# Kernel tuning notes

Measured on AMD Instinct MI355X. Metric: run time of the kernel, lower is better.

## Reference

```python
import jax, jax.numpy as jnp
import numpy as np

IN_CH = 512
HID_CH = 512
NUM_HEADS = HID_CH // 32  # 16 heads, 32 channels each
GN_GROUPS = 32
EPS = 1e-6


def group_norm(x, scale, bias):
    # x: (b, c, t); GroupNorm over (channels-in-group, t)
    b, c, t = x.shape
    xg = x.reshape(b, GN_GROUPS, c // GN_GROUPS, t)
    mean = xg.mean(axis=(2, 3), keepdims=True)
    var = xg.var(axis=(2, 3), keepdims=True)
    xg = (xg - mean) * jax.lax.rsqrt(var + EPS)
    return xg.reshape(b, c, t) * scale[None, :, None] + bias[None, :, None]


def setup_inputs() -> dict:
    key = jax.random.key(0)
    ks = jax.random.split(key, 12)
    b, t = 16, 8192
    s = 0.02
    return {
        "x": jax.random.normal(ks[0], (b, IN_CH, t), dtype=jnp.float32),
        "gn_scale": jnp.ones((IN_CH,), jnp.float32),
        "gn_bias": jnp.zeros((IN_CH,), jnp.float32),
        "wq": jax.random.normal(ks[1], (HID_CH, IN_CH), jnp.float32) * s,
        "bq": jnp.zeros((HID_CH,), jnp.float32),
        "wk": jax.random.normal(ks[2], (HID_CH, IN_CH), jnp.float32) * s,
        "bk": jnp.zeros((HID_CH,), jnp.float32),
        "wv": jax.random.normal(ks[3], (HID_CH, IN_CH), jnp.float32) * s,
        "bv": jnp.zeros((HID_CH,), jnp.float32),
        "wp": jax.random.normal(ks[4], (IN_CH, HID_CH), jnp.float32) * s,
        "bp": jnp.zeros((IN_CH,), jnp.float32),
    }


def reference(x, gn_scale, gn_bias, wq, bq, wk, bk, wv, bv, wp, bp):
    b, _, t = x.shape
    n = NUM_HEADS
    hc = HID_CH // n  # 32 channels per head
    h = group_norm(x, gn_scale, gn_bias)
    # 1x1 conv == channel GEMM: (b,c_in,t) -> (b,c_out,t)
    q = jnp.einsum('oc,bct->bot', wq, h) + bq[None, :, None]
    k = jnp.einsum('oc,bct->bot', wk, h) + bk[None, :, None]
    v = jnp.einsum('oc,bct->bot', wv, h) + bv[None, :, None]
    q = q.reshape(b, n, hc, t)
    k = k.reshape(b, n, hc, t)
    v = v.reshape(b, n, hc, t)
    # q: softmax over channel dim; k: rearranged to (.., t, c), softmax over c
    q = jax.nn.softmax(q, axis=2)          # (b,n,c,t), softmax over c
    k = jax.nn.softmax(k, axis=2)          # softmax over c (dim=-1 after b n t c rearrange)
    w = jnp.einsum('bnct,bndt->bncd', q, k)   # (b,n,c,c) small cxc matrix
    h = jnp.einsum('bncd,bndt->bnct', w, v)   # (b,n,c,t)
    h = h.reshape(b, HID_CH, t)
    out = jnp.einsum('oc,bct->bot', wp, h) + bp[None, :, None]
    return x + out
```

## Files before the change

kernel.cpp:

```cpp
#include <hip/hip_runtime.h>

typedef _Float16 f16;
typedef _Float16 f16x8 __attribute__((ext_vector_type(8)));
typedef float f32x4 __attribute__((ext_vector_type(4)));
typedef float f32x16 __attribute__((ext_vector_type(16)));


__device__ __forceinline__ void gl_lds16(const f16* g, const void* lds) {
    __builtin_amdgcn_global_load_lds((const __attribute__((address_space(1))) void*)g,
                                     (__attribute__((address_space(3))) void*)lds, 16, 0, 0);
}

__global__ __launch_bounds__(256) void k_tr(const float* __restrict__ x, f16* __restrict__ xT,
                                            float* __restrict__ part,
                                            const float* __restrict__ wv, f16* __restrict__ WvT) {
    int tid = threadIdx.x;
    if (blockIdx.x >= 16384) {
        int idx = (blockIdx.x - 16384) * 256 + tid;
        int c = idx >> 9, e = idx & 511;
        WvT[idx] = (f16)wv[(size_t)e * 512 + c];
        return;
    }
    __shared__ f16 ldsT[64][72];
    int tt = blockIdx.x & 127, ct = (blockIdx.x >> 7) & 7, b = blockIdx.x >> 10;
    int cc = tid >> 2, tq = tid & 3;
    int c = ct * 64 + cc;
    const float* xp = x + ((size_t)b * 512 + c) * 8192 + tt * 64 + tq * 16;
    float s = 0.f, s2 = 0.f;
#pragma unroll
    for (int q4 = 0; q4 < 4; ++q4) {
        f32x4 v = *(const f32x4*)(xp + q4 * 4);
#pragma unroll
        for (int j = 0; j < 4; ++j) {
            ldsT[tq * 16 + q4 * 4 + j][cc] = (f16)v[j];
            s += v[j]; s2 += v[j] * v[j];
        }
    }
#pragma unroll
    for (int k = 1; k < 64; k <<= 1) { s += __shfl_xor(s, k); s2 += __shfl_xor(s2, k); }
    if ((tid & 63) == 0) {
        float* pp = part + (((size_t)b * 32 + ct * 4 + (tid >> 6)) * 128 + tt) * 2;
        pp[0] = s; pp[1] = s2;
    }
    __syncthreads();
    int tl = tid >> 2, cq = tid & 3;
    f16x8 v0 = *(const f16x8*)(&ldsT[tl][cq * 16]);
    f16x8 v1 = *(const f16x8*)(&ldsT[tl][cq * 16 + 8]);
    f16* hp = xT + ((size_t)b * 8192 + tt * 64 + tl) * 512 + ct * 64 + cq * 16;
    *(f16x8*)(hp) = v0;
    *(f16x8*)(hp + 8) = v1;
}

__global__ __launch_bounds__(512) void k_stats2(const float* __restrict__ part, float* __restrict__ stats) {
    int i = threadIdx.x;
    const float* pp = part + (size_t)i * 256;
    float s = 0.f, s2 = 0.f;
    for (int t = 0; t < 128; ++t) { s += pp[t * 2]; s2 += pp[t * 2 + 1]; }
    float mean = s * (1.f / 131072.f);
    float var  = s2 * (1.f / 131072.f) - mean * mean;
    stats[i * 2 + 0] = mean;
    stats[i * 2 + 1] = rsqrtf(var + 1e-6f);
}

__global__ __launch_bounds__(256) void k_prep(const float* __restrict__ wq, const float* __restrict__ wk,
                                              const float* __restrict__ wv,
                                              const float* __restrict__ gsc, const float* __restrict__ gbi,
                                              const float* __restrict__ stats,
                                              const float* __restrict__ bq, const float* __restrict__ bk,
                                              f16* __restrict__ Wqkp2, float* __restrict__ qkb,
                                              float* __restrict__ u) {
    __shared__ float scn[512], bi[512], red[256];
    int tid = threadIdx.x;
    int blk = blockIdx.x;
    int b = (blk < 256) ? (blk >> 4) : ((blk - 256) >> 3);
    for (int i = tid; i < 512; i += 256) {
        float mean = stats[(b * 32 + (i >> 4)) * 2 + 0];
        float rstd = stats[(b * 32 + (i >> 4)) * 2 + 1];
        float sc = gsc[i] * rstd;
        scn[i] = sc;
        bi[i] = gbi[i] - mean * sc;
    }
    __syncthreads();
    if (blk < 256) {
        int rg = blk & 15;
        int pr = rg * 64 + (tid >> 2);
        int cq = tid & 3;
        int hg = pr >> 8, ri = pr & 255;
        int hl = ri >> 6, qk = (ri >> 5) & 1, ch = ri & 31;
        int src = (hg * 4 + hl) * 32 + ch;
        const float* wrow = (qk ? wk : wq) + (size_t)src * 512;
        f16* orow = Wqkp2 + ((size_t)b * 1024 + pr) * 512;
        float dot = 0.f;
        for (int c0 = cq * 128; c0 < cq * 128 + 128; c0 += 8) {
            f16x8 o8;
#pragma unroll
            for (int j = 0; j < 8; ++j) {
                float wv_ = wrow[c0 + j] * scn[c0 + j];
                o8[j] = (f16)wv_;
                dot += wv_ * bi[c0 + j];
            }
            *(f16x8*)(orow + c0) = o8;
        }
        red[tid] = dot;
        __syncthreads();
        if (cq == 0)
            qkb[(size_t)b * 1024 + pr] = red[tid] + red[tid + 1] + red[tid + 2] + red[tid + 3]
                                         + (qk ? bk[src] : bq[src]);
    } else {
        int ug = (blk - 256) & 7;
        int e = ug * 64 + (tid >> 2);
        int cq = tid & 3;
        const float* wrow = wv + (size_t)e * 512;
        float dot = 0.f;
        for (int c = cq * 128; c < cq * 128 + 128; ++c) dot += wrow[c] * bi[c];
        red[tid] = dot;
        __syncthreads();
        if (cq == 0) u[(size_t)b * 512 + e] = red[tid] + red[tid + 1] + red[tid + 2] + red[tid + 3];
    }
}

__device__ __forceinline__ void gemm_core(const f16* __restrict__ Abase, int lda,
                                          const f16* __restrict__ Bbase,
                                          char* smem, int tid, f32x4 acc[4][4]) {
    const int lane = tid & 63, wave = tid >> 6;
    const int wm = wave >> 1, wn = wave & 1;
    char* As = smem;
    char* Bs = smem + 16384;
    const int srow = (lane >> 3);
    const int schunk = (lane & 7) ^ srow;
    for (int kt = 0; kt < 8; ++kt) {
#pragma unroll
        for (int i = 0; i < 4; ++i) {
            int row = (wave * 4 + i) * 8 + srow;
            gl_lds16(Abase + (size_t)row * lda + kt * 64 + schunk * 8, As + (wave * 4 + i) * 1024);
            gl_lds16(Bbase + (size_t)row * 512 + kt * 64 + schunk * 8, Bs + (wave * 4 + i) * 1024);
        }
        __syncthreads();
#pragma unroll
        for (int ks = 0; ks < 2; ++ks) {
            f16x8 af[4], bf[4];
#pragma unroll
            for (int i = 0; i < 4; ++i) {
                int row = wm * 64 + i * 16 + (lane & 15);
                int ch = (ks * 4 + (lane >> 4)) ^ (lane & 7);
                af[i] = *(const f16x8*)(As + row * 128 + ch * 16);
            }
#pragma unroll
            for (int j = 0; j < 4; ++j) {
                int row = wn * 64 + j * 16 + (lane & 15);
                int ch = (ks * 4 + (lane >> 4)) ^ (lane & 7);
                bf[j] = *(const f16x8*)(Bs + row * 128 + ch * 16);
            }
#pragma unroll
            for (int i = 0; i < 4; ++i)
#pragma unroll
                for (int j = 0; j < 4; ++j)
                    acc[i][j] = __builtin_amdgcn_mfma_f32_16x16x32_f16(af[i], bf[j], acc[i][j], 0, 0, 0);
        }
        __syncthreads();
    }
}

__global__ __launch_bounds__(256, 2) void k_qk_w(const f16* __restrict__ xT, const f16* __restrict__ Wqkp2,
                                                 const float* __restrict__ qkb, float* __restrict__ w_part) {
    __shared__ __align__(16) char smem[49152];
    int tid = threadIdx.x, lane = tid & 63, wave = tid >> 6;
    int bid = blockIdx.x;
    int lb = (bid & 7) * 512 + (bid >> 3);
    int batch = lb >> 8;
    int rem = lb & 255;
    int tt = rem >> 2, hg = rem & 3;
    const f16* Abase = Wqkp2 + ((size_t)batch * 1024 + hg * 256) * 512;
    const f16* Bbase = xT + ((size_t)batch * 8192 + (size_t)tt * 128) * 512;
    char* As = smem;
    char* Bs = smem + 32768;
    const int srow = lane >> 3;
    const int schunk = (lane & 7) ^ srow;
    f32x4 acc[4][8];
#pragma unroll
    for (int i = 0; i < 4; ++i)
#pragma unroll
        for (int j = 0; j < 8; ++j) acc[i][j] = (f32x4){0.f, 0.f, 0.f, 0.f};

    for (int kt = 0; kt < 8; ++kt) {
#pragma unroll
        for (int i = 0; i < 8; ++i) {
            int g = wave * 8 + i;
            gl_lds16(Abase + (size_t)(g * 8 + srow) * 512 + kt * 64 + schunk * 8, As + g * 1024);
        }
#pragma unroll
        for (int i = 0; i < 4; ++i) {
            int g = wave * 4 + i;
            gl_lds16(Bbase + (size_t)(g * 8 + srow) * 512 + kt * 64 + schunk * 8, Bs + g * 1024);
        }
        __syncthreads();
#pragma unroll
        for (int ks = 0; ks < 2; ++ks) {
            f16x8 af[4];
#pragma unroll
            for (int i = 0; i < 4; ++i) {
                int row = wave * 64 + i * 16 + (lane & 15);
                int ch = (ks * 4 + (lane >> 4)) ^ (lane & 7);
                af[i] = *(const f16x8*)(As + row * 128 + ch * 16);
            }
#pragma unroll
            for (int j = 0; j < 8; ++j) {
                int row = j * 16 + (lane & 15);
                int ch = (ks * 4 + (lane >> 4)) ^ (lane & 7);
                f16x8 bf = *(const f16x8*)(Bs + row * 128 + ch * 16);
#pragma unroll
                for (int i = 0; i < 4; ++i)
                    acc[i][j] = __builtin_amdgcn_mfma_f32_16x16x32_f16(af[i], bf, acc[i][j], 0, 0, 0);
            }
        }
        __syncthreads();
    }

    float qb[2][8];
#pragma unroll
    for (int qk = 0; qk < 2; ++qk)
#pragma unroll
        for (int i2 = 0; i2 < 2; ++i2)
#pragma unroll
            for (int r = 0; r < 4; ++r)
                qb[qk][i2 * 4 + r] = qkb[(size_t)batch * 1024 + hg * 256 + wave * 64 + qk * 32 +
                                         i2 * 16 + (lane >> 4) * 4 + r];
    f16* qbuf = (f16*)(smem + wave * 9216);
    f16* kbuf = qbuf + 32 * 72;
    f32x16 wacc;
#pragma unroll
    for (int i = 0; i < 16; ++i) wacc[i] = 0.f;

#pragma unroll
    for (int th = 0; th < 2; ++th) {
#pragma unroll
        for (int jl = 0; jl < 4; ++jl) {
            int j = th * 4 + jl;
#pragma unroll
            for (int qk = 0; qk < 2; ++qk) {
                int ib = qk * 2;
                float v0[8];
#pragma unroll
                for (int i2 = 0; i2 < 2; ++i2)
#pragma unroll
                    for (int r = 0; r < 4; ++r)
                        v0[i2 * 4 + r] = acc[ib + i2][j][r] + qb[qk][i2 * 4 + r];
                float mx = v0[0];
#pragma unroll
                for (int i = 1; i < 8; ++i) mx = fmaxf(mx, v0[i]);
                mx = fmaxf(mx, __shfl_xor(mx, 16));
                mx = fmaxf(mx, __shfl_xor(mx, 32));
                float s = 0.f;
#pragma unroll
                for (int i = 0; i < 8; ++i) { v0[i] = __expf(v0[i] - mx); s += v0[i]; }
                s += __shfl_xor(s, 16);
                s += __shfl_xor(s, 32);
                float inv = 1.f / s;
                f16* dst = qk ? kbuf : qbuf;
                int tcol = jl * 16 + (lane & 15);
#pragma unroll
                for (int i2 = 0; i2 < 2; ++i2)
#pragma unroll
                    for (int r = 0; r < 4; ++r) {
                        int c = i2 * 16 + (lane >> 4) * 4 + r;
                        dst[c * 72 + tcol] = (f16)(v0[i2 * 4 + r] * inv);
                    }
            }
        }
#pragma unroll
        for (int ks = 0; ks < 4; ++ks) {
            f16x8 a  = *(const f16x8*)(qbuf + (lane & 31) * 72 + ks * 16 + (lane >> 5) * 8);
            f16x8 bb = *(const f16x8*)(kbuf + (lane & 31) * 72 + ks * 16 + (lane >> 5) * 8);
            wacc = __builtin_amdgcn_mfma_f32_32x32x16_f16(a, bb, wacc, 0, 0, 0);
        }
    }
    int ghead = hg * 4 + wave;
    float* wpo = w_part + (((size_t)tt * 16 + batch) * 16 + ghead) * 1024;
#pragma unroll
    for (int r = 0; r < 16; ++r) {
        int row = (r & 3) + 8 * (r >> 2) + 4 * (lane >> 5);
        wpo[row * 32 + (lane & 31)] = wacc[r];
    }
}

__global__ __launch_bounds__(256) void k_wreduce(const float* __restrict__ w_part, float* __restrict__ w_red) {
    int blk = blockIdx.x;
    int tid = threadIdx.x;
    f32x4 s = (f32x4){0.f, 0.f, 0.f, 0.f};
    for (int tt = 0; tt < 64; ++tt) {
        f32x4 v = *(const f32x4*)(w_part + ((size_t)tt * 256 + blk) * 1024 + tid * 4);
        s += v;
    }
    *(f32x4*)(w_red + (size_t)blk * 1024 + tid * 4) = s;
}

__global__ __launch_bounds__(256) void k_wpe(const float* __restrict__ w_red, const float* __restrict__ wp,
                                             const float* __restrict__ bv, const float* __restrict__ u,
                                             const float* __restrict__ bp,
                                             f16* __restrict__ wpe, float* __restrict__ bias_p) {
    __shared__ float wl[16384];
    __shared__ float bred[256];
    int tid = threadIdx.x;
    int b = blockIdx.x >> 3, ot = blockIdx.x & 7;
    for (int idx = tid; idx < 16384; idx += 256) wl[idx] = w_red[(size_t)b * 16384 + idx];
    __syncthreads();
    int o = ot * 64 + (tid >> 2);
    int cq = tid & 3;
    float bacc = 0.f;
#pragma unroll
    for (int ng = 0; ng < 4; ++ng) {
        int n = cq * 4 + ng;
        float a[32];
#pragma unroll
        for (int d = 0; d < 32; ++d) a[d] = 0.f;
        for (int e = 0; e < 32; ++e) {
            float wv = wp[(size_t)o * 512 + n * 32 + e];
#pragma unroll
            for (int d = 0; d < 32; ++d) a[d] += wv * wl[n * 1024 + e * 32 + d];
        }
#pragma unroll
        for (int dc = 0; dc < 4; ++dc) {
            f16x8 o8;
#pragma unroll
            for (int j = 0; j < 8; ++j) o8[j] = (f16)a[dc * 8 + j];
            *(f16x8*)(wpe + ((size_t)b * 512 + o) * 512 + n * 32 + dc * 8) = o8;
        }
#pragma unroll
        for (int d = 0; d < 32; ++d) bacc += a[d] * (bv[n * 32 + d] + u[(size_t)b * 512 + n * 32 + d]);
    }
    bred[tid] = bacc;
    __syncthreads();
    if ((tid & 3) == 0)
        bias_p[(size_t)b * 512 + o] = bp[o] + bred[tid] + bred[tid + 1] + bred[tid + 2] + bred[tid + 3];
}

__global__ __launch_bounds__(256) void k_wfin(const f16* __restrict__ wpe, const f16* __restrict__ WvT,
                                              const float* __restrict__ gsc, const float* __restrict__ stats,
                                              f16* __restrict__ Wfin) {
    __shared__ __align__(16) char smem[34816];
    int tid = threadIdx.x, lane = tid & 63, wave = tid >> 6;
    int wm = wave >> 1, wn = wave & 1;
    int bid = blockIdx.x;
    int b = bid >> 4, mt = (bid >> 2) & 3, nt = bid & 3;
    const f16* Abase = wpe + (size_t)b * 262144 + (size_t)mt * 128 * 512;
    const f16* Bbase = WvT + (size_t)nt * 128 * 512;
    f32x4 acc[4][4];
#pragma unroll
    for (int i = 0; i < 4; ++i)
#pragma unroll
        for (int j = 0; j < 4; ++j) acc[i][j] = (f32x4){0.f, 0.f, 0.f, 0.f};
    gemm_core(Abase, 512, Bbase, smem, tid, acc);
    float scnj[4];
#pragma unroll
    for (int j = 0; j < 4; ++j) {
        int col = nt * 128 + wn * 64 + j * 16 + (lane & 15);
        scnj[j] = gsc[col] * stats[(b * 32 + (col >> 4)) * 2 + 1];
    }
    f16* epi = (f16*)smem;
#pragma unroll
    for (int i = 0; i < 4; ++i)
#pragma unroll
        for (int j = 0; j < 4; ++j)
#pragma unroll
            for (int r = 0; r < 4; ++r) {
                int m = wm * 64 + i * 16 + (lane >> 4) * 4 + r;
                int n = wn * 64 + j * 16 + (lane & 15);
                epi[m * 136 + n] = (f16)(acc[i][j][r] * scnj[j]);
            }
    __syncthreads();
#pragma unroll
    for (int rr = 0; rr < 8; ++rr) {
        int row = wave * 32 + (lane >> 4) * 8 + rr;
        f16x8 vv = *(const f16x8*)(epi + row * 136 + (lane & 15) * 8);
        *(f16x8*)(Wfin + (size_t)b * 262144 + (size_t)(mt * 128 + row) * 512 + nt * 128 + (lane & 15) * 8) = vv;
    }
}

__global__ __launch_bounds__(256, 2) void k_out(const f16* __restrict__ xT, const f16* __restrict__ Wfin,
                                                const float* __restrict__ x, const float* __restrict__ bias_p,
                                                float* __restrict__ out) {
    __shared__ __align__(16) char smem[49152];
    int tid = threadIdx.x, lane = tid & 63, wave = tid >> 6;
    int bid = blockIdx.x;
    int lb = (bid & 7) * 256 + (bid >> 3);
    int batch = lb >> 7;
    int rem = lb & 127;
    int tt = rem >> 1, ot2 = rem & 1;
    const f16* Abase = Wfin + (size_t)batch * 262144 + (size_t)ot2 * 256 * 512;
    const f16* Bbase = xT + ((size_t)batch * 8192 + (size_t)tt * 128) * 512;
    char* As = smem;
    char* Bs = smem + 32768;
    const int srow = lane >> 3;
    const int schunk = (lane & 7) ^ srow;
    f32x4 acc[4][8];
#pragma unroll
    for (int i = 0; i < 4; ++i)
#pragma unroll
        for (int j = 0; j < 8; ++j) acc[i][j] = (f32x4){0.f, 0.f, 0.f, 0.f};

    for (int kt = 0; kt < 8; ++kt) {
#pragma unroll
        for (int i = 0; i < 8; ++i) {
            int g = wave * 8 + i;
            gl_lds16(Abase + (size_t)(g * 8 + srow) * 512 + kt * 64 + schunk * 8, As + g * 1024);
        }
#pragma unroll
        for (int i = 0; i < 4; ++i) {
            int g = wave * 4 + i;
            gl_lds16(Bbase + (size_t)(g * 8 + srow) * 512 + kt * 64 + schunk * 8, Bs + g * 1024);
        }
        __syncthreads();
#pragma unroll
        for (int ks = 0; ks < 2; ++ks) {
            f16x8 af[4];
#pragma unroll
            for (int i = 0; i < 4; ++i) {
                int row = wave * 64 + i * 16 + (lane & 15);
                int ch = (ks * 4 + (lane >> 4)) ^ (lane & 7);
                af[i] = *(const f16x8*)(As + row * 128 + ch * 16);
            }
#pragma unroll
            for (int j = 0; j < 8; ++j) {
                int row = j * 16 + (lane & 15);
                int ch = (ks * 4 + (lane >> 4)) ^ (lane & 7);
                f16x8 bf = *(const f16x8*)(Bs + row * 128 + ch * 16);
#pragma unroll
                for (int i = 0; i < 4; ++i)
                    acc[i][j] = __builtin_amdgcn_mfma_f32_16x16x32_f16(af[i], bf, acc[i][j], 0, 0, 0);
            }
        }
        __syncthreads();
    }

    float* ep = (float*)smem;
    const int orow_in = (lane >> 4) * 4;
    for (int ow = 0; ow < 4; ++ow) {
        __syncthreads();
        if (wave == ow) {
#pragma unroll
            for (int i = 0; i < 4; ++i)
#pragma unroll
                for (int j = 0; j < 8; ++j)
#pragma unroll
                    for (int r = 0; r < 4; ++r)
                        ep[(i * 16 + orow_in + r) * 132 + j * 16 + (lane & 15)] = acc[i][j][r];
        }
        __syncthreads();
        int o_g0 = ot2 * 256 + ow * 64;
#pragma unroll
        for (int p = 0; p < 8; ++p) {
            int idx = p * 256 + tid;
            int row = idx >> 5;
            int tq = (idx & 31) * 4;
            int o = o_g0 + row;
            float bpv = bias_p[batch * 512 + o];
            size_t g = ((size_t)batch * 512 + o) * 8192 + (size_t)tt * 128 + tq;
            f32x4 xv = *(const f32x4*)(x + g);
            f32x4 lv = *(const f32x4*)(ep + row * 132 + tq);
            f32x4 ov;
#pragma unroll
            for (int j = 0; j < 4; ++j) ov[j] = xv[j] + bpv + lv[j];
            *(f32x4*)(out + g) = ov;
        }
    }
}

extern "C" void kernel_launch(void* const* d_in, const int* in_sizes, int n_in,
                              void* d_out, int out_size, void* d_ws, size_t ws_size,
                              hipStream_t stream) {
    const float* x   = (const float*)d_in[0];
    const float* gsc = (const float*)d_in[1];
    const float* gbi = (const float*)d_in[2];
    const float* wq  = (const float*)d_in[3];
    const float* bq  = (const float*)d_in[4];
    const float* wk  = (const float*)d_in[5];
    const float* bk  = (const float*)d_in[6];
    const float* wv  = (const float*)d_in[7];
    const float* bv  = (const float*)d_in[8];
    const float* wp  = (const float*)d_in[9];
    const float* bp  = (const float*)d_in[10];
    float* out = (float*)d_out;
    char* ws = (char*)d_ws;

    size_t o_stats = 0;
    size_t o_part  = 4096;
    size_t o_qkb   = o_part + 524288;
    size_t o_u     = o_qkb + 65536;
    size_t o_biasp = o_u + 32768;
    size_t o_wvt   = o_biasp + 32768;
    size_t o_wred  = o_wvt + 524288;
    size_t o_wpe   = o_wred + 1048576;
    size_t o_wfin  = o_wpe + 8388608;
    size_t o_wqkp2 = o_wfin + 8388608;
    size_t o_wpart = o_wqkp2 + 16777216;
    size_t o_xT    = o_wpart + 67108864;
    size_t total   = o_xT + 134217728;
    if (ws_size < total) return;

    float* stats  = (float*)(ws + o_stats);
    float* part   = (float*)(ws + o_part);
    float* qkb    = (float*)(ws + o_qkb);
    float* u      = (float*)(ws + o_u);
    float* bias_p = (float*)(ws + o_biasp);
    f16*   WvT    = (f16*)(ws + o_wvt);
    float* w_red  = (float*)(ws + o_wred);
    f16*   wpe    = (f16*)(ws + o_wpe);
    f16*   Wfin   = (f16*)(ws + o_wfin);
    f16*   Wqkp2  = (f16*)(ws + o_wqkp2);
    float* w_part = (float*)(ws + o_wpart);
    f16*   xT     = (f16*)(ws + o_xT);

    k_tr     <<<17408, 256, 0, stream>>>(x, xT, part, wv, WvT);
    k_stats2 <<<1,     512, 0, stream>>>(part, stats);
    k_prep   <<<384,   256, 0, stream>>>(wq, wk, wv, gsc, gbi, stats, bq, bk, Wqkp2, qkb, u);
    k_qk_w   <<<4096,  256, 0, stream>>>(xT, Wqkp2, qkb, w_part);
    k_wreduce<<<256,   256, 0, stream>>>(w_part, w_red);
    k_wpe    <<<128,   256, 0, stream>>>(w_red, wp, bv, u, bp, wpe, bias_p);
    k_wfin   <<<256,   256, 0, stream>>>(wpe, WvT, gsc, stats, Wfin);
    k_out    <<<2048,  256, 0, stream>>>(xT, Wfin, x, bias_p, out);
}
```

Before: 517.8 us.

## Fuse GN stats into prep, store W partials in fp16, halve epilogue passes

Removes the single-block k_stats2 launch by having each k_prep block reduce its own batch's GroupNorm partials, with a subset of blocks writing stats for later kernels. Partial 32x32 attention-weight matrices are stored in fp16 instead of fp32, halving the write and reduce traffic. The k_out epilogue stages accumulators in LDS as fp16, so two waves share a pass and the number of sync rounds drops from four to two. This adds fp16 rounding to the partial w sums and the output projection, and every prep block now repeats the stats reduction.

```diff
diff --git a/kernel.cpp b/kernel.cpp
--- a/kernel.cpp
+++ b/kernel.cpp
@@ -2,6 +2,7 @@
 
 typedef _Float16 f16;
 typedef _Float16 f16x8 __attribute__((ext_vector_type(8)));
+typedef _Float16 f16x4 __attribute__((ext_vector_type(4)));
 typedef float f32x4 __attribute__((ext_vector_type(4)));
 typedef float f32x16 __attribute__((ext_vector_type(16)));
 
@@ -51,34 +52,44 @@
     *(f16x8*)(hp + 8) = v1;
 }
 
-__global__ __launch_bounds__(512) void k_stats2(const float* __restrict__ part, float* __restrict__ stats) {
-    int i = threadIdx.x;
-    const float* pp = part + (size_t)i * 256;
-    float s = 0.f, s2 = 0.f;
-    for (int t = 0; t < 128; ++t) { s += pp[t * 2]; s2 += pp[t * 2 + 1]; }
-    float mean = s * (1.f / 131072.f);
-    float var  = s2 * (1.f / 131072.f) - mean * mean;
-    stats[i * 2 + 0] = mean;
-    stats[i * 2 + 1] = rsqrtf(var + 1e-6f);
-}
-
 __global__ __launch_bounds__(256) void k_prep(const float* __restrict__ wq, const float* __restrict__ wk,
                                               const float* __restrict__ wv,
                                               const float* __restrict__ gsc, const float* __restrict__ gbi,
-                                              const float* __restrict__ stats,
+                                              const float* __restrict__ part,
                                               const float* __restrict__ bq, const float* __restrict__ bk,
                                               f16* __restrict__ Wqkp2, float* __restrict__ qkb,
-                                              float* __restrict__ u) {
+                                              float* __restrict__ u, float* __restrict__ stats) {
     __shared__ float scn[512], bi[512], red[256];
     int tid = threadIdx.x;
     int blk = blockIdx.x;
     int b = (blk < 256) ? (blk >> 4) : ((blk - 256) >> 3);
+    {
+        int g = tid >> 3, ch = tid & 7;
+        const float* pp = part + (((size_t)b * 32 + g) * 128 + ch * 16) * 2;
+        float s = 0.f, s2 = 0.f;
+        for (int t2 = 0; t2 < 16; ++t2) { s += pp[t2 * 2]; s2 += pp[t2 * 2 + 1]; }
+        scn[tid] = s; bi[tid] = s2;
+    }
+    __syncthreads();
+    if (tid < 32) {
+        float S = 0.f, S2 = 0.f;
+#pragma unroll
+        for (int j = 0; j < 8; ++j) { S += scn[tid * 8 + j]; S2 += bi[tid * 8 + j]; }
+        float mean = S * (1.f / 131072.f);
+        float var  = S2 * (1.f / 131072.f) - mean * mean;
+        float rstd = rsqrtf(var + 1e-6f);
+        red[tid] = mean;
+        red[128 + tid] = rstd;
+        if (blk >= 256 && ((blk - 256) & 7) == 0) {
+            stats[(b * 32 + tid) * 2 + 0] = mean;
+            stats[(b * 32 + tid) * 2 + 1] = rstd;
+        }
+    }
+    __syncthreads();
     for (int i = tid; i < 512; i += 256) {
-        float mean = stats[(b * 32 + (i >> 4)) * 2 + 0];
-        float rstd = stats[(b * 32 + (i >> 4)) * 2 + 1];
-        float sc = gsc[i] * rstd;
+        float sc = gsc[i] * red[128 + (i >> 4)];
         scn[i] = sc;
-        bi[i] = gbi[i] - mean * sc;
+        bi[i] = gbi[i] - red[i >> 4] * sc;
     }
     __syncthreads();
     if (blk < 256) {
@@ -162,7 +173,7 @@
 }
 
 __global__ __launch_bounds__(256, 2) void k_qk_w(const f16* __restrict__ xT, const f16* __restrict__ Wqkp2,
-                                                 const float* __restrict__ qkb, float* __restrict__ w_part) {
+                                                 const float* __restrict__ qkb, f16* __restrict__ w_part) {
     __shared__ __align__(16) char smem[49152];
     int tid = threadIdx.x, lane = tid & 63, wave = tid >> 6;
     int bid = blockIdx.x;
@@ -275,21 +286,22 @@
         }
     }
     int ghead = hg * 4 + wave;
-    float* wpo = w_part + (((size_t)tt * 16 + batch) * 16 + ghead) * 1024;
+    f16* wpo = w_part + (((size_t)tt * 16 + batch) * 16 + ghead) * 1024;
 #pragma unroll
     for (int r = 0; r < 16; ++r) {
         int row = (r & 3) + 8 * (r >> 2) + 4 * (lane >> 5);
-        wpo[row * 32 + (lane & 31)] = wacc[r];
-    }
-}
-
-__global__ __launch_bounds__(256) void k_wreduce(const float* __restrict__ w_part, float* __restrict__ w_red) {
+        wpo[row * 32 + (lane & 31)] = (f16)wacc[r];
+    }
+}
+
+__global__ __launch_bounds__(256) void k_wreduce(const f16* __restrict__ w_part, float* __restrict__ w_red) {
     int blk = blockIdx.x;
     int tid = threadIdx.x;
     f32x4 s = (f32x4){0.f, 0.f, 0.f, 0.f};
     for (int tt = 0; tt < 64; ++tt) {
-        f32x4 v = *(const f32x4*)(w_part + ((size_t)tt * 256 + blk) * 1024 + tid * 4);
-        s += v;
+        f16x4 v = *(const f16x4*)(w_part + ((size_t)tt * 256 + blk) * 1024 + tid * 4);
+#pragma unroll
+        for (int j = 0; j < 4; ++j) s[j] += (float)v[j];
     }
     *(f32x4*)(w_red + (size_t)blk * 1024 + tid * 4) = s;
 }
@@ -432,23 +444,24 @@
         __syncthreads();
     }
 
-    float* ep = (float*)smem;
+    f16* ep = (f16*)smem;
     const int orow_in = (lane >> 4) * 4;
-    for (int ow = 0; ow < 4; ++ow) {
-        __syncthreads();
-        if (wave == ow) {
+    for (int pp = 0; pp < 2; ++pp) {
+        __syncthreads();
+        if ((wave >> 1) == pp) {
+            f16* myep = ep + (size_t)(wave & 1) * 64 * 132;
 #pragma unroll
             for (int i = 0; i < 4; ++i)
 #pragma unroll
                 for (int j = 0; j < 8; ++j)
 #pragma unroll
                     for (int r = 0; r < 4; ++r)
-                        ep[(i * 16 + orow_in + r) * 132 + j * 16 + (lane & 15)] = acc[i][j][r];
-        }
-        __syncthreads();
-        int o_g0 = ot2 * 256 + ow * 64;
-#pragma unroll
-        for (int p = 0; p < 8; ++p) {
+                        myep[(i * 16 + orow_in + r) * 132 + j * 16 + (lane & 15)] = (f16)acc[i][j][r];
+        }
+        __syncthreads();
+        int o_g0 = ot2 * 256 + pp * 128;
+#pragma unroll
+        for (int p = 0; p < 16; ++p) {
             int idx = p * 256 + tid;
             int row = idx >> 5;
             int tq = (idx & 31) * 4;
@@ -456,10 +469,10 @@
             float bpv = bias_p[batch * 512 + o];
             size_t g = ((size_t)batch * 512 + o) * 8192 + (size_t)tt * 128 + tq;
             f32x4 xv = *(const f32x4*)(x + g);
-            f32x4 lv = *(const f32x4*)(ep + row * 132 + tq);
+            f16x4 lv = *(const f16x4*)(ep + row * 132 + tq);
             f32x4 ov;
 #pragma unroll
-            for (int j = 0; j < 4; ++j) ov[j] = xv[j] + bpv + lv[j];
+            for (int j = 0; j < 4; ++j) ov[j] = xv[j] + bpv + (float)lv[j];
             *(f32x4*)(out + g) = ov;
         }
     }
@@ -493,7 +506,7 @@
     size_t o_wfin  = o_wpe + 8388608;
     size_t o_wqkp2 = o_wfin + 8388608;
     size_t o_wpart = o_wqkp2 + 16777216;
-    size_t o_xT    = o_wpart + 67108864;
+    size_t o_xT    = o_wpart + 33554432;
     size_t total   = o_xT + 134217728;
     if (ws_size < total) return;
 
@@ -507,12 +520,11 @@
     f16*   wpe    = (f16*)(ws + o_wpe);
     f16*   Wfin   = (f16*)(ws + o_wfin);
     f16*   Wqkp2  = (f16*)(ws + o_wqkp2);
-    float* w_part = (float*)(ws + o_wpart);
+    f16*   w_part = (f16*)(ws + o_wpart);
     f16*   xT     = (f16*)(ws + o_xT);
 
     k_tr     <<<17408, 256, 0, stream>>>(x, xT, part, wv, WvT);
-    k_stats2 <<<1,     512, 0, stream>>>(part, stats);
-    k_prep   <<<384,   256, 0, stream>>>(wq, wk, wv, gsc, gbi, stats, bq, bk, Wqkp2, qkb, u);
+    k_prep   <<<384,   256, 0, stream>>>(wq, wk, wv, gsc, gbi, part, bq, bk, Wqkp2, qkb, u, stats);
     k_qk_w   <<<4096,  256, 0, stream>>>(xT, Wqkp2, qkb, w_part);
     k_wreduce<<<256,   256, 0, stream>>>(w_part, w_red);
     k_wpe    <<<128,   256, 0, stream>>>(w_red, wp, bv, u, bp, wpe, bias_p);
```

After: 494.2 us, median of 2. 4.5% less time.
